# Optimization experiments

Hardware: AMD Instinct MI355X
Metric: run time of the kernel (lower is better)

## Reference

```python
import jax, jax.numpy as jnp
import numpy as np

GROUPS = 32
EPS = 1e-5


def group_norm(x, w, b):
    B, C, H, W = x.shape
    xg = x.reshape(B, GROUPS, C // GROUPS, H, W)
    mu = xg.mean(axis=(2, 3, 4), keepdims=True)
    var = xg.var(axis=(2, 3, 4), keepdims=True)
    xg = (xg - mu) * jax.lax.rsqrt(var + EPS)
    return xg.reshape(B, C, H, W) * w[None, :, None, None] + b[None, :, None, None]


def conv1x1(x, w, b):
    # 1x1 conv == per-position GEMM over channels
    return jnp.einsum('bchw,dc->bdhw', x, w) + b[None, :, None, None]


def setup_inputs() -> dict:
    key = jax.random.key(0)
    ks = jax.random.split(key, 8)
    B, C, H, W = 16, 512, 32, 32
    scale = C ** -0.5  # keep pre-softmax logits well-conditioned
    return {
        'x': jax.random.normal(ks[0], (B, C, H, W), jnp.float32),
        'temb': jax.random.normal(ks[1], (B, C), jnp.float32),
        'gn_w': jnp.ones((C,), jnp.float32),
        'gn_b': jnp.zeros((C,), jnp.float32),
        'q_w': jax.random.normal(ks[2], (C, C), jnp.float32) * scale,
        'q_b': jnp.zeros((C,), jnp.float32),
        'k_w': jax.random.normal(ks[3], (C, C), jnp.float32) * scale,
        'k_b': jnp.zeros((C,), jnp.float32),
        'v_w': jax.random.normal(ks[4], (C, C), jnp.float32) * scale,
        'v_b': jnp.zeros((C,), jnp.float32),
        'p_w': jax.random.normal(ks[5], (C, C), jnp.float32) * scale,
        'p_b': jnp.zeros((C,), jnp.float32),
    }


def reference(x, temb, gn_w, gn_b, q_w, q_b, k_w, k_b, v_w, v_b, p_w, p_b):
    B, C, H, W = x.shape
    h = group_norm(x, gn_w, gn_b)
    q = conv1x1(h, q_w, q_b)
    k = conv1x1(h, k_w, k_b)
    v = conv1x1(h, v_w, v_b)
    # spatial self-attention: every (h,w) query attends over all (H,W) keys
    scores = jnp.einsum('bchw,bcHW->bhwHW', q, k) * (C ** -0.5)  # [B,H,W,H,W]
    attn = jax.nn.softmax(scores.reshape(B, H, W, H * W), axis=-1).reshape(B, H, W, H, W)
    h = jnp.einsum('bhwHW,bcHW->bchw', attn, v)
    return x + conv1x1(h, p_w, p_b)
```

## Files before the change

kernel.cpp:

```cpp
#include <hip/hip_runtime.h>

typedef unsigned short u16;
typedef __bf16 bf16x8 __attribute__((ext_vector_type(8)));
typedef float f32x4 __attribute__((ext_vector_type(4)));
typedef unsigned short u16x8 __attribute__((ext_vector_type(8)));

__device__ __forceinline__ u16 f2bf(float f) {
  unsigned u = __builtin_bit_cast(unsigned, f);
  u += 0x7fffu + ((u >> 16) & 1u);
  return (u16)(u >> 16);
}
__device__ __forceinline__ float b2f(u16 h) {
  return __builtin_bit_cast(float, (unsigned)h << 16);
}

__device__ __forceinline__ void gld16(const u16* g, u16* l) {
  __builtin_amdgcn_global_load_lds((const __attribute__((address_space(1))) unsigned int*)g,
                                   (__attribute__((address_space(3))) unsigned int*)l, 16, 0, 0);
}

#define GN_ROW 1026

__global__ __launch_bounds__(256) void gncvt_kernel(
    const float* __restrict__ x, const float* __restrict__ w, const float* __restrict__ bias,
    u16* __restrict__ hn,
    const float* __restrict__ qw, const float* __restrict__ kw, const float* __restrict__ vw,
    const float* __restrict__ pw, const float* __restrict__ qb, const float* __restrict__ kb,
    u16* __restrict__ wqk, u16* __restrict__ wv, u16* __restrict__ wp, float* __restrict__ qkb,
    float scale) {
  const int tid = threadIdx.x;
  if (blockIdx.x >= 512) {
    const int j = blockIdx.x - 512;
    const int yy = j >> 8, xx = j & 255;
    if (yy == 4) {
      int i = xx * 256 + tid;
      if (i < 512) qkb[i] = qb[i] * scale;
      else if (i < 1024) qkb[i] = kb[i - 512];
      return;
    }
    const float* s;
    u16* o;
    float sc = 1.f;
    switch (yy) {
      case 0: s = qw; o = wqk; sc = scale; break;
      case 1: s = kw; o = wqk + 262144; break;
      case 2: s = vw; o = wv; break;
      default: s = pw; o = wp; break;
    }
    int i = (xx * 256 + tid) * 4;
    float4 v = *(const float4*)(s + i);
    ushort4 pk = { f2bf(v.x * sc), f2bf(v.y * sc), f2bf(v.z * sc), f2bf(v.w * sc) };
    *(ushort4*)&o[i] = pk;
    return;
  }

  __shared__ u16 tile[16 * GN_ROW];
  __shared__ float red[18];
  const int bb = blockIdx.x & 15;
  const int g = blockIdx.x >> 4;
  const float4* xb = (const float4*)(x + ((size_t)bb * 512 + (size_t)g * 16) * 1024);

  float s = 0.f, sq = 0.f;
#pragma unroll
  for (int j = 0; j < 16; ++j) {
    float4 v = xb[j * 256 + tid];
    s += v.x + v.y + v.z + v.w;
    sq += v.x * v.x + v.y * v.y + v.z * v.z + v.w * v.w;
    int base = j * GN_ROW + tid * 4;
    ushort2 p0 = { f2bf(v.x), f2bf(v.y) };
    ushort2 p1 = { f2bf(v.z), f2bf(v.w) };
    *(ushort2*)&tile[base] = p0;
    *(ushort2*)&tile[base + 2] = p1;
  }
#pragma unroll
  for (int o = 32; o; o >>= 1) {
    s += __shfl_down(s, o, 64);
    sq += __shfl_down(sq, o, 64);
  }
  const int wv_ = tid >> 6;
  if ((tid & 63) == 0) { red[wv_] = s; red[wv_ + 4] = sq; }
  __syncthreads();
  if (tid == 0) {
    float S = red[0] + red[1] + red[2] + red[3];
    float Q = red[4] + red[5] + red[6] + red[7];
    float mean = S * (1.f / 16384.f);
    float var = Q * (1.f / 16384.f) - mean * mean;
    red[16] = mean;
    red[17] = rsqrtf(var + 1e-5f);
  }
  __syncthreads();
  const float mean = red[16], rstd = red[17];
  const int c0 = g * 16;

  float wf[16], bf_[16];
#pragma unroll
  for (int c = 0; c < 16; ++c) {
    float wc = w[c0 + c];
    wf[c] = wc * rstd;
    bf_[c] = bias[c0 + c] - mean * rstd * wc;
  }
#pragma unroll
  for (int it = 0; it < 4; ++it) {
    int hw = it * 256 + tid;
    u16x8 lo{}, hi{};
#pragma unroll
    for (int c = 0; c < 8; ++c) {
      lo[c] = f2bf(b2f(tile[c * GN_ROW + hw]) * wf[c] + bf_[c]);
      hi[c] = f2bf(b2f(tile[(c + 8) * GN_ROW + hw]) * wf[c + 8] + bf_[c + 8]);
    }
    u16* dst = hn + ((size_t)bb * 1024 + hw) * 512 + c0;
    *(u16x8*)dst = lo;
    *(u16x8*)(dst + 8) = hi;
  }
}

template <int BM, int BN, int TPB, int MINW, typename OutT>
__global__ __launch_bounds__(TPB, MINW) void gemm_nt(
    const u16* __restrict__ A, const u16* __restrict__ Bt, OutT* __restrict__ C,
    const float* __restrict__ bias_m, const float* __restrict__ bias_n, const float* __restrict__ res,
    int K, int lda, int ldb, int ldc, size_t sA, size_t sB, size_t sC, size_t sRes,
    int T, int lognbx) {
  constexpr int NW = TPB / 64;
  constexpr int WGN = BN / 64;
  constexpr int WGM = NW / WGN;
  constexpr int WTM = BM / WGM;
  constexpr int MT = WTM / 16;
  constexpr int ASLOT = 8 * BM / TPB;
  constexpr int BSLOT = 8 * BN / TPB;
  __shared__ u16 lsA[2][BM * 64];
  __shared__ u16 lsB[2][BN * 64];

  int fi = blockIdx.x;
  const int halfT = T << 3;
  const int h = (fi >= halfT);
  fi -= h * halfT;
  const int tile = fi >> 3;
  const int zb = (fi & 7) + (h << 3);
  const int bx = tile & ((1 << lognbx) - 1);
  const int by = tile >> lognbx;

  const int tid = threadIdx.x;
  const int lane = tid & 63;
  const int wave = tid >> 6;
  const int wm = wave / WGN, wn = wave % WGN;
  const int tm = by * BM, tn = bx * BN;
  const u16* Ab = A + (size_t)zb * sA;
  const u16* Bb = Bt + (size_t)zb * sB;

  f32x4 acc[MT][4] = {};
  const int q = lane >> 4, r = lane & 15;

  const u16* pA[ASLOT];
  const u16* pB[BSLOT];
#pragma unroll
  for (int i = 0; i < ASLOT; ++i) {
    int e = tid + i * TPB;
    int ra = e >> 3, sl = e & 7;
    int g = sl ^ ((ra >> 1) & 7);
    pA[i] = Ab + (size_t)(tm + ra) * lda + g * 8;
  }
#pragma unroll
  for (int i = 0; i < BSLOT; ++i) {
    int e = tid + i * TPB;
    int ra = e >> 3, sl = e & 7;
    int g = sl ^ ((ra >> 1) & 7);
    pB[i] = Bb + (size_t)(tn + ra) * ldb + g * 8;
  }

#pragma unroll
  for (int i = 0; i < ASLOT; ++i) gld16(pA[i], &lsA[0][(tid + i * TPB) * 8]);
#pragma unroll
  for (int i = 0; i < BSLOT; ++i) gld16(pB[i], &lsB[0][(tid + i * TPB) * 8]);
  __syncthreads();

  int offA[MT][2], offB[4][2];
#pragma unroll
  for (int mt = 0; mt < MT; ++mt) {
    int rowa = wm * WTM + mt * 16 + r;
#pragma unroll
    for (int ks = 0; ks < 2; ++ks)
      offA[mt][ks] = rowa * 64 + ((ks * 4 + q) ^ ((rowa >> 1) & 7)) * 8;
  }
#pragma unroll
  for (int nt = 0; nt < 4; ++nt) {
    int rowb = wn * 64 + nt * 16 + r;
#pragma unroll
    for (int ks = 0; ks < 2; ++ks)
      offB[nt][ks] = rowb * 64 + ((ks * 4 + q) ^ ((rowb >> 1) & 7)) * 8;
  }

  const int nk = K >> 6;
  for (int k = 0; k < nk; ++k) {
    const int cur = k & 1;
    if (k + 1 < nk) {
      const int k0 = (k + 1) << 6;
#pragma unroll
      for (int i = 0; i < ASLOT; ++i) gld16(pA[i] + k0, &lsA[cur ^ 1][(tid + i * TPB) * 8]);
#pragma unroll
      for (int i = 0; i < BSLOT; ++i) gld16(pB[i] + k0, &lsB[cur ^ 1][(tid + i * TPB) * 8]);
    }
#pragma unroll
    for (int ks = 0; ks < 2; ++ks) {
      bf16x8 af[MT], bfv[4];
#pragma unroll
      for (int mt = 0; mt < MT; ++mt) af[mt] = *(const bf16x8*)(const void*)&lsA[cur][offA[mt][ks]];
#pragma unroll
      for (int nt = 0; nt < 4; ++nt) bfv[nt] = *(const bf16x8*)(const void*)&lsB[cur][offB[nt][ks]];
#pragma unroll
      for (int mt = 0; mt < MT; ++mt)
#pragma unroll
        for (int nt = 0; nt < 4; ++nt)
          acc[mt][nt] = __builtin_amdgcn_mfma_f32_16x16x32_bf16(af[mt], bfv[nt], acc[mt][nt], 0, 0, 0);
    }
    __syncthreads();
  }

  OutT* Cb = C + (size_t)zb * sC;
  const float* Rb = res ? res + (size_t)zb * sRes : nullptr;
#pragma unroll
  for (int mt = 0; mt < MT; ++mt) {
#pragma unroll
    for (int nt = 0; nt < 4; ++nt) {
      const int col = tn + wn * 64 + nt * 16 + r;
      const float bn = bias_n ? bias_n[col] : 0.f;
#pragma unroll
      for (int reg = 0; reg < 4; ++reg) {
        const int row = tm + wm * WTM + mt * 16 + q * 4 + reg;
        float v = acc[mt][nt][reg];
        const float bm = bias_m ? bias_m[row] : 0.f;
        v = v + bm + bn;
        const size_t idx = (size_t)row * ldc + col;
        if (Rb) v += Rb[idx];
        if constexpr (__is_same(OutT, u16)) Cb[idx] = f2bf(v);
        else Cb[idx] = v;
      }
    }
  }
}

__global__ __launch_bounds__(512, 2) void gemm_pv(const u16* __restrict__ S, const u16* __restrict__ V,
                                                  u16* __restrict__ O) {
  __shared__ u16 lsA[2][256 * 64];
  __shared__ u16 lsB[2][128 * 64];
  __shared__ float psum[2048];
  __shared__ float sinv[256];

  int fi = blockIdx.x;
  const int h = (fi >= 128);
  fi -= h * 128;
  const int tile = fi >> 3;
  const int zb = (fi & 7) + (h << 3);
  const int bx = tile & 3;
  const int by = tile >> 2;

  const int tid = threadIdx.x;
  const int lane = tid & 63;
  const int wave = tid >> 6;
  const int wm = wave >> 1, wn = wave & 1;
  const int tm = by * 256, tn = bx * 128;
  const u16* Ab = S + (size_t)zb * 1048576;
  const u16* Bb = V + (size_t)zb * 524288;

  const u16* pa[4];
  const u16* pb[2];
  int laoff[4], lboff[2];
#pragma unroll
  for (int i = 0; i < 4; ++i) {
    int e = tid + i * 512;
    int ra = e >> 3, sl = e & 7;
    int g = sl ^ ((ra >> 1) & 7);
    pa[i] = Ab + (size_t)(tm + ra) * 1024 + g * 8;
    laoff[i] = e * 8;
  }
#pragma unroll
  for (int i = 0; i < 2; ++i) {
    int e = tid + i * 512;
    int rb = e >> 3, sl = e & 7;
    int g = sl ^ ((rb >> 1) & 7);
    pb[i] = Bb + (size_t)(tn + rb) * 1024 + g * 8;
    lboff[i] = e * 8;
  }

  float ps[4] = {0.f, 0.f, 0.f, 0.f};

#pragma unroll
  for (int i = 0; i < 4; ++i) {
    u16x8 a0 = *(const u16x8*)pa[i];
    u16x8 t0;
    float loc = 0.f;
#pragma unroll
    for (int t = 0; t < 8; ++t) {
      float e_ = __expf(b2f(a0[t]));
      loc += e_;
      t0[t] = f2bf(e_);
    }
    ps[i] += loc;
    *(u16x8*)&lsA[0][laoff[i]] = t0;
  }
#pragma unroll
  for (int i = 0; i < 2; ++i) gld16(pb[i], &lsB[0][lboff[i]]);
  __syncthreads();

  const int q = lane >> 4, r = lane & 15;
  int offA[4][2], offB[4][2];
#pragma unroll
  for (int mt = 0; mt < 4; ++mt) {
    int rowa = wm * 64 + mt * 16 + r;
    int rowb = wn * 64 + mt * 16 + r;
#pragma unroll
    for (int ks = 0; ks < 2; ++ks) {
      offA[mt][ks] = rowa * 64 + ((ks * 4 + q) ^ ((rowa >> 1) & 7)) * 8;
      offB[mt][ks] = rowb * 64 + ((ks * 4 + q) ^ ((rowb >> 1) & 7)) * 8;
    }
  }

  f32x4 acc[4][4] = {};
  const int nk = 16;
  for (int k = 0; k < nk; ++k) {
    const int cur = k & 1;
    u16x8 an[4];
    if (k + 1 < nk) {
      const int k0 = (k + 1) << 6;
#pragma unroll
      for (int i = 0; i < 4; ++i) an[i] = *(const u16x8*)(pa[i] + k0);
#pragma unroll
      for (int i = 0; i < 2; ++i) gld16(pb[i] + k0, &lsB[cur ^ 1][lboff[i]]);
    }
#pragma unroll
    for (int ks = 0; ks < 2; ++ks) {
      bf16x8 af[4], bfv[4];
#pragma unroll
      for (int mt = 0; mt < 4; ++mt) af[mt] = *(const bf16x8*)(const void*)&lsA[cur][offA[mt][ks]];
#pragma unroll
      for (int nt = 0; nt < 4; ++nt) bfv[nt] = *(const bf16x8*)(const void*)&lsB[cur][offB[nt][ks]];
#pragma unroll
      for (int mt = 0; mt < 4; ++mt)
#pragma unroll
        for (int nt = 0; nt < 4; ++nt)
          acc[mt][nt] = __builtin_amdgcn_mfma_f32_16x16x32_bf16(af[mt], bfv[nt], acc[mt][nt], 0, 0, 0);
    }
    if (k + 1 < nk) {
#pragma unroll
      for (int i = 0; i < 4; ++i) {
        u16x8 t8;
        float loc = 0.f;
#pragma unroll
        for (int t = 0; t < 8; ++t) {
          float e_ = __expf(b2f(an[i][t]));
          loc += e_;
          t8[t] = f2bf(e_);
        }
        ps[i] += loc;
        *(u16x8*)&lsA[cur ^ 1][laoff[i]] = t8;
      }
    }
    __syncthreads();
  }

#pragma unroll
  for (int i = 0; i < 4; ++i) psum[tid + i * 512] = ps[i];
  __syncthreads();
  if (tid < 256) {
    float s = 0.f;
#pragma unroll
    for (int j = 0; j < 8; ++j) s += psum[tid * 8 + j];
    sinv[tid] = 1.f / s;
  }
  __syncthreads();

  u16* Ob = O + (size_t)zb * 524288;
#pragma unroll
  for (int mt = 0; mt < 4; ++mt) {
#pragma unroll
    for (int nt = 0; nt < 4; ++nt) {
      const int col = tn + wn * 64 + nt * 16 + r;
#pragma unroll
      for (int reg = 0; reg < 4; ++reg) {
        const int lrow = wm * 64 + mt * 16 + q * 4 + reg;
        Ob[(size_t)(tm + lrow) * 512 + col] = f2bf(acc[mt][nt][reg] * sinv[lrow]);
      }
    }
  }
}

extern "C" void kernel_launch(void* const* d_in, const int* in_sizes, int n_in,
                              void* d_out, int out_size, void* d_ws, size_t ws_size,
                              hipStream_t stream) {
  const float* x = (const float*)d_in[0];
  const float* gn_w = (const float*)d_in[2];
  const float* gn_b = (const float*)d_in[3];
  const float* q_w = (const float*)d_in[4];
  const float* q_b = (const float*)d_in[5];
  const float* k_w = (const float*)d_in[6];
  const float* k_b = (const float*)d_in[7];
  const float* v_w = (const float*)d_in[8];
  const float* v_b = (const float*)d_in[9];
  const float* p_w = (const float*)d_in[10];
  const float* p_b = (const float*)d_in[11];
  float* out = (float*)d_out;

  u16* wqk = (u16*)d_ws;
  u16* wv = wqk + 524288;
  u16* wp = wv + 262144;
  float* qkb = (float*)(wp + 262144);
  u16* hn = wp + 262144 + 2048;
  u16* qkt = hn + 8388608;
  u16* vv = qkt + 16777216;
  u16* ot = vv + 8388608;
  u16* Sb = ot + 8388608;

  const float inv_sqrt_c = 0.044194173824159216f;
  const size_t sHN = 524288, sS = 1048576;

  gncvt_kernel<<<1792, 256, 0, stream>>>(x, gn_w, gn_b, hn, q_w, k_w, v_w, p_w, q_b, k_b,
                                         wqk, wv, wp, qkb, inv_sqrt_c);

  gemm_nt<256, 256, 1024, 4, u16><<<256, 1024, 0, stream>>>(hn, wqk, qkt, nullptr, qkb, nullptr,
                                                            512, 512, 512, 1024, sHN, 0, sS, 0, 16, 2);
  gemm_nt<256, 128, 512, 2, u16><<<256, 512, 0, stream>>>(wv, hn, vv, v_b, nullptr, nullptr,
                                                          512, 512, 512, 1024, 0, sHN, sHN, 0, 16, 3);
  gemm_nt<256, 256, 1024, 4, u16><<<256, 1024, 0, stream>>>(qkt, qkt + 512, Sb, nullptr, nullptr, nullptr,
                                                            512, 1024, 1024, 1024, sS, sS, sS, 0, 16, 2);
  gemm_pv<<<256, 512, 0, stream>>>(Sb, vv, ot);
  gemm_nt<256, 128, 512, 2, float><<<256, 512, 0, stream>>>(wp, ot, out, p_b, nullptr, x,
                                                            512, 512, 512, 1024, 0, sHN, sHN, sHN, 16, 3);
}
```

Measured before the change: 247.5 us.

## Fuse QK and V projection GEMMs into one smaller-tile launch

Replaces the two separate projection GEMM launches (QK with 256x256 tiles, V with 256x128 tiles) with one kernel using 128x128 tiles, 256 threads and a 32-wide K step. Blocks are split by index between the QK and V problems. This removes one launch and the tail gap between the two, and gives 1536 smaller blocks for better CU fill. The cost is lower per-block data reuse, a simple two-stage pipeline, and scalar bf16 stores in the epilogue that may coalesce poorly.

```diff
diff --git a/kernel.cpp b/kernel.cpp
--- a/kernel.cpp
+++ b/kernel.cpp
@@ -114,6 +114,111 @@
   }
 }
 
+__global__ __launch_bounds__(256, 2) void qkv_kernel(
+    const u16* __restrict__ hn, const u16* __restrict__ wqk, const u16* __restrict__ wv,
+    u16* __restrict__ qkt, u16* __restrict__ vv,
+    const float* __restrict__ qkb, const float* __restrict__ v_b) {
+  __shared__ u16 lsA[2][4096];
+  __shared__ u16 lsB[2][4096];
+  const int bid = blockIdx.x;
+  const int z = bid & 15;
+  const int t = bid >> 4;
+  const int tid = threadIdx.x;
+  const int lane = tid & 63, wave = tid >> 6;
+  const int wm = wave >> 1, wn = wave & 1;
+  const int q = lane >> 4, r = lane & 15;
+
+  const u16* Ab;
+  const u16* Bb;
+  u16* Cb;
+  const float* bm;
+  const float* bn;
+  int tm, tn;
+  if (t < 64) {
+    Ab = hn + (size_t)z * 524288;
+    Bb = wqk;
+    Cb = qkt + (size_t)z * 1048576;
+    bm = nullptr;
+    bn = qkb;
+    tm = (t >> 3) * 128;
+    tn = (t & 7) * 128;
+  } else {
+    const int t2 = t - 64;
+    Ab = wv;
+    Bb = hn + (size_t)z * 524288;
+    Cb = vv + (size_t)z * 524288;
+    bm = v_b;
+    bn = nullptr;
+    tm = (t2 >> 3) * 128;
+    tn = (t2 & 7) * 128;
+  }
+
+  const u16* pA[2];
+  const u16* pB[2];
+#pragma unroll
+  for (int i = 0; i < 2; ++i) {
+    int e = tid + i * 256;
+    int ra = e >> 2, sl = e & 3;
+    int g = sl ^ ((ra >> 1) & 3);
+    pA[i] = Ab + (size_t)(tm + ra) * 512 + g * 8;
+    pB[i] = Bb + (size_t)(tn + ra) * 512 + g * 8;
+  }
+#pragma unroll
+  for (int i = 0; i < 2; ++i) gld16(pA[i], &lsA[0][(tid + i * 256) * 8]);
+#pragma unroll
+  for (int i = 0; i < 2; ++i) gld16(pB[i], &lsB[0][(tid + i * 256) * 8]);
+  __syncthreads();
+
+  int offA[4], offB[4];
+#pragma unroll
+  for (int mt = 0; mt < 4; ++mt) {
+    int rowa = wm * 64 + mt * 16 + r;
+    offA[mt] = rowa * 32 + (q ^ ((rowa >> 1) & 3)) * 8;
+    int rowb = wn * 64 + mt * 16 + r;
+    offB[mt] = rowb * 32 + (q ^ ((rowb >> 1) & 3)) * 8;
+  }
+
+  f32x4 acc[4][4] = {};
+  const int nk = 16;
+  for (int k = 0; k < nk; ++k) {
+    const int cur = k & 1;
+    if (k + 1 < nk) {
+      const int k0 = (k + 1) << 5;
+#pragma unroll
+      for (int i = 0; i < 2; ++i) gld16(pA[i] + k0, &lsA[cur ^ 1][(tid + i * 256) * 8]);
+#pragma unroll
+      for (int i = 0; i < 2; ++i) gld16(pB[i] + k0, &lsB[cur ^ 1][(tid + i * 256) * 8]);
+    }
+    bf16x8 af[4], bfv[4];
+#pragma unroll
+    for (int mt = 0; mt < 4; ++mt) {
+      af[mt] = *(const bf16x8*)(const void*)&lsA[cur][offA[mt]];
+      bfv[mt] = *(const bf16x8*)(const void*)&lsB[cur][offB[mt]];
+    }
+#pragma unroll
+    for (int mt = 0; mt < 4; ++mt)
+#pragma unroll
+      for (int nt = 0; nt < 4; ++nt)
+        acc[mt][nt] = __builtin_amdgcn_mfma_f32_16x16x32_bf16(af[mt], bfv[nt], acc[mt][nt], 0, 0, 0);
+    __syncthreads();
+  }
+
+#pragma unroll
+  for (int mt = 0; mt < 4; ++mt) {
+#pragma unroll
+    for (int nt = 0; nt < 4; ++nt) {
+      const int col = tn + wn * 64 + nt * 16 + r;
+      const float bnv = bn ? bn[col] : 0.f;
+#pragma unroll
+      for (int reg = 0; reg < 4; ++reg) {
+        const int row = tm + wm * 64 + mt * 16 + q * 4 + reg;
+        const float bmv = bm ? bm[row] : 0.f;
+        Cb[(size_t)row * 1024 + col] = f2bf(acc[mt][nt][reg] + bmv + bnv);
+      }
+    }
+  }
+}
+
 template <int BM, int BN, int TPB, int MINW, typename OutT>
 __global__ __launch_bounds__(TPB, MINW) void gemm_nt(
     const u16* __restrict__ A, const u16* __restrict__ Bt, OutT* __restrict__ C,
@@ -415,10 +520,8 @@
   gncvt_kernel<<<1792, 256, 0, stream>>>(x, gn_w, gn_b, hn, q_w, k_w, v_w, p_w, q_b, k_b,
                                          wqk, wv, wp, qkb, inv_sqrt_c);
 
-  gemm_nt<256, 256, 1024, 4, u16><<<256, 1024, 0, stream>>>(hn, wqk, qkt, nullptr, qkb, nullptr,
-                                                            512, 512, 512, 1024, sHN, 0, sS, 0, 16, 2);
-  gemm_nt<256, 128, 512, 2, u16><<<256, 512, 0, stream>>>(wv, hn, vv, v_b, nullptr, nullptr,
-                                                          512, 512, 512, 1024, 0, sHN, sHN, 0, 16, 3);
+  qkv_kernel<<<1536, 256, 0, stream>>>(hn, wqk, wv, qkt, vv, qkb, v_b);
+
   gemm_nt<256, 256, 1024, 4, u16><<<256, 1024, 0, stream>>>(qkt, qkt + 512, Sb, nullptr, nullptr, nullptr,
                                                             512, 1024, 1024, 1024, sS, sS, sS, 0, 16, 2);
   gemm_pv<<<256, 512, 0, stream>>>(Sb, vv, ot);
```

Result: no change. 250.2 us (+1.1%).

## Add 8-wave 256x256 GEMM with 4-stage LDS pipeline for QK and scores

Applied to the files above, without the earlier changes.

Adds a gemm8 kernel that computes a 256x256 tile with 512 threads (8 waves, each owning a 128x64 sub-tile) instead of 1024 threads. It uses a 4-slot LDS ring with K-step 32, issues global-to-LDS loads interleaved with MFMA phases, uses swizzled LDS offsets, and raises wave priority around the MFMA bursts. It replaces the QK projection and score GEMMs. The aim is better latency hiding and more work per wave. In exchange each wave holds a larger accumulator set, which raises register pressure and issues more barriers per K-step.

```diff
diff --git a/kernel.cpp b/kernel.cpp
--- a/kernel.cpp
+++ b/kernel.cpp
@@ -114,6 +114,138 @@
   }
 }
 
+template <typename OutT>
+__global__ __launch_bounds__(512, 2) void gemm8(
+    const u16* __restrict__ A, const u16* __restrict__ Bt, OutT* __restrict__ C,
+    const float* __restrict__ bias_m, const float* __restrict__ bias_n,
+    int K, int lda, int ldb, int ldc, size_t sA, size_t sB, size_t sC,
+    int T, int lognbx) {
+  constexpr int ASZ = 256 * 32;
+  constexpr int SLOT = 2 * ASZ;
+  __shared__ u16 ls[4 * SLOT];
+
+  int fi = blockIdx.x;
+  const int halfT = T << 3;
+  const int h = (fi >= halfT);
+  fi -= h * halfT;
+  const int tile = fi >> 3;
+  const int zb = (fi & 7) + (h << 3);
+  const int bx = tile & ((1 << lognbx) - 1);
+  const int by = tile >> lognbx;
+
+  const int tid = threadIdx.x;
+  const int lane = tid & 63;
+  const int wave = tid >> 6;
+  const int wm = wave >> 2, wn = wave & 3;
+  const int tm = by * 256, tn = bx * 256;
+  const u16* Ab = A + (size_t)zb * sA;
+  const u16* Bb = Bt + (size_t)zb * sB;
+  const int q = lane >> 4, r = lane & 15;
+
+  const u16* pA[2];
+  const u16* pB[2];
+  int aoff[2], boff[2];
+#pragma unroll
+  for (int i = 0; i < 2; ++i) {
+    int e = tid + i * 512;
+    int ra = e >> 2, sl = e & 3;
+    int g = sl ^ ((ra >> 1) & 3);
+    pA[i] = Ab + (size_t)(tm + ra) * lda + g * 8;
+    pB[i] = Bb + (size_t)(tn + ra) * ldb + g * 8;
+    aoff[i] = e * 8;
+    boff[i] = ASZ + e * 8;
+  }
+
+  int offA[8], offB[4];
+#pragma unroll
+  for (int mt = 0; mt < 8; ++mt) {
+    int rowa = wm * 128 + mt * 16 + r;
+    offA[mt] = rowa * 32 + (q ^ ((rowa >> 1) & 3)) * 8;
+  }
+#pragma unroll
+  for (int nt = 0; nt < 4; ++nt) {
+    int rowb = wn * 64 + nt * 16 + r;
+    offB[nt] = ASZ + rowb * 32 + (q ^ ((rowb >> 1) & 3)) * 8;
+  }
+
+  const int nk = K >> 5;
+
+#pragma unroll
+  for (int t = 0; t < 3; ++t) {
+    u16* S = ls + t * SLOT;
+    const int k0 = t << 5;
+#pragma unroll
+    for (int i = 0; i < 2; ++i) gld16(pA[i] + k0, &S[aoff[i]]);
+#pragma unroll
+    for (int i = 0; i < 2; ++i) gld16(pB[i] + k0, &S[boff[i]]);
+  }
+  asm volatile("s_waitcnt vmcnt(8)" ::: "memory");
+  __builtin_amdgcn_s_barrier();
+
+  f32x4 acc[8][4] = {};
+
+  for (int t = 0; t < nk; ++t) {
+    const u16* cs = ls + (t & 3) * SLOT;
+    u16* SS = ls + ((t + 3) & 3) * SLOT;
+    const bool st = (t + 3) < nk;
+    const int k0 = (t + 3) << 5;
+#pragma unroll
+    for (int p = 0; p < 4; ++p) {
+      const int mh = p >> 1, nh = p & 1;
+      bf16x8 af[4], bf2[2];
+#pragma unroll
+      for (int m = 0; m < 4; ++m) af[m] = *(const bf16x8*)(const void*)&cs[offA[mh * 4 + m]];
+#pragma unroll
+      for (int n = 0; n < 2; ++n) bf2[n] = *(const bf16x8*)(const void*)&cs[offB[nh * 2 + n]];
+      if (st) {
+        if (p == 0) gld16(pA[0] + k0, &SS[aoff[0]]);
+        else if (p == 1) gld16(pA[1] + k0, &SS[aoff[1]]);
+        else if (p == 2) gld16(pB[0] + k0, &SS[boff[0]]);
+        else gld16(pB[1] + k0, &SS[boff[1]]);
+      }
+      if (p == 3) {
+        if (t + 3 < nk) {
+          asm volatile("s_waitcnt vmcnt(8)" ::: "memory");
+        } else if (t + 2 < nk) {
+          asm volatile("s_waitcnt vmcnt(4)" ::: "memory");
+        } else {
+          asm volatile("s_waitcnt vmcnt(0)" ::: "memory");
+        }
+      }
+      __builtin_amdgcn_s_barrier();
+      __builtin_amdgcn_s_setprio(1);
+#pragma unroll
+      for (int m = 0; m < 4; ++m)
+#pragma unroll
+        for (int n = 0; n < 2; ++n)
+          acc[mh * 4 + m][nh * 2 + n] =
+              __builtin_amdgcn_mfma_f32_16x16x32_bf16(af[m], bf2[n], acc[mh * 4 + m][nh * 2 + n], 0, 0, 0);
+      __builtin_amdgcn_s_setprio(0);
+      __builtin_amdgcn_s_barrier();
+    }
+  }
+
+  OutT* Cb = C + (size_t)zb * sC;
+#pragma unroll
+  for (int mt = 0; mt < 8; ++mt) {
+#pragma unroll
+    for (int nt = 0; nt < 4; ++nt) {
+      const int col = tn + wn * 64 + nt * 16 + r;
+      const float bn = bias_n ? bias_n[col] : 0.f;
+#pragma unroll
+      for (int reg = 0; reg < 4; ++reg) {
+        const int row = tm + wm * 128 + mt * 16 + q * 4 + reg;
+        float v = acc[mt][nt][reg];
+        const float bm = bias_m ? bias_m[row] : 0.f;
+        v = v + bm + bn;
+        const size_t idx = (size_t)row * ldc + col;
+        if constexpr (__is_same(OutT, u16)) Cb[idx] = f2bf(v);
+        else Cb[idx] = v;
+      }
+    }
+  }
+}
+
 template <int BM, int BN, int TPB, int MINW, typename OutT>
 __global__ __launch_bounds__(TPB, MINW) void gemm_nt(
     const u16* __restrict__ A, const u16* __restrict__ Bt, OutT* __restrict__ C,
@@ -415,12 +547,12 @@
   gncvt_kernel<<<1792, 256, 0, stream>>>(x, gn_w, gn_b, hn, q_w, k_w, v_w, p_w, q_b, k_b,
                                          wqk, wv, wp, qkb, inv_sqrt_c);
 
-  gemm_nt<256, 256, 1024, 4, u16><<<256, 1024, 0, stream>>>(hn, wqk, qkt, nullptr, qkb, nullptr,
-                                                            512, 512, 512, 1024, sHN, 0, sS, 0, 16, 2);
+  gemm8<u16><<<256, 512, 0, stream>>>(hn, wqk, qkt, nullptr, qkb,
+                                      512, 512, 512, 1024, sHN, 0, sS, 16, 2);
   gemm_nt<256, 128, 512, 2, u16><<<256, 512, 0, stream>>>(wv, hn, vv, v_b, nullptr, nullptr,
                                                           512, 512, 512, 1024, 0, sHN, sHN, 0, 16, 3);
-  gemm_nt<256, 256, 1024, 4, u16><<<256, 1024, 0, stream>>>(qkt, qkt + 512, Sb, nullptr, nullptr, nullptr,
-                                                            512, 1024, 1024, 1024, sS, sS, sS, 0, 16, 2);
+  gemm8<u16><<<256, 512, 0, stream>>>(qkt, qkt + 512, Sb, nullptr, nullptr,
+                                      512, 1024, 1024, 1024, sS, sS, sS, 16, 2);
   gemm_pv<<<256, 512, 0, stream>>>(Sb, vv, ot);
   gemm_nt<256, 128, 512, 2, float><<<256, 512, 0, stream>>>(wp, ot, out, p_b, nullptr, x,
                                                             512, 512, 512, 1024, 0, sHN, sHN, sHN, 16, 3);
```

Measured after the change: 275.5 us. +11.3%, slower.
